# Optimization experiments

Measured on AMD Instinct MI355X. Metric: run time of the kernel, lower is better.

The kernel has to match this reference:

```python
import jax, jax.numpy as jnp
import numpy as np

N, S, D_MODEL, H = 2, 2048, 1024, 16
HEAD_DIM = D_MODEL // H


def setup_inputs() -> dict:
    key = jax.random.key(0)
    k1, k2, k3 = jax.random.split(key, 3)
    x = jax.random.normal(k1, (N, S, D_MODEL), dtype=jnp.float32)
    # Xavier-uniform-like scaling for the projection weights (torch layout: [out, in])
    lim_qkv = (6.0 / (D_MODEL + 3 * D_MODEL)) ** 0.5
    lim_o = (6.0 / (D_MODEL + D_MODEL)) ** 0.5
    qkv_w = jax.random.uniform(k2, (3 * D_MODEL, D_MODEL), dtype=jnp.float32, minval=-lim_qkv, maxval=lim_qkv)
    o_w = jax.random.uniform(k3, (D_MODEL, D_MODEL), dtype=jnp.float32, minval=-lim_o, maxval=lim_o)
    return {"x": x, "qkv_w": qkv_w, "o_w": o_w}


def reference(x, qkv_w, o_w):
    n, s, _ = x.shape
    # qkv projection (torch Linear: y = x @ W^T), no bias
    qkv = jnp.einsum("nsd,ed->nse", x, qkv_w)            # (N, S, 3*D_MODEL)
    qkv = qkv.reshape(n, s, H, 3 * HEAD_DIM).transpose(0, 2, 1, 3)  # (N, H, S, 3*hd)
    q, k, v = jnp.split(qkv, 3, axis=-1)                 # each (N, H, S, hd)
    scale = 1.0 / jnp.sqrt(jnp.float32(HEAD_DIM))
    attn_logits = jnp.einsum("nhqd,nhkd->nhqk", q, k) * scale  # (N, H, S, S)
    attn_weights = jax.nn.softmax(attn_logits, axis=-1)
    values = jnp.einsum("nhqk,nhkd->nhqd", attn_weights, v)    # (N, H, S, hd)
    values = values.transpose(0, 2, 1, 3).reshape(n, s, D_MODEL)
    o = jnp.einsum("nsd,ed->nse", values, o_w)           # (N, S, D_MODEL)
    return o
```

## Files before the change

### kernel.cpp

```cpp
#include <hip/hip_runtime.h>
#include <math.h>

#define H 16
#define S 2048
#define DM 1024
#define HD 64
#define QSCALE 0.18033688011112042f

typedef __attribute__((ext_vector_type(8))) short short8;
typedef __attribute__((ext_vector_type(4))) float f32x4;
typedef __attribute__((ext_vector_type(4))) unsigned short u16x4;
typedef __attribute__((ext_vector_type(2))) unsigned int uint2v;
#if __has_builtin(__builtin_amdgcn_cvt_pk_bf16_f32)
typedef __attribute__((ext_vector_type(2))) __bf16 bf16x2;
#endif

__device__ __forceinline__ unsigned short f2bf(float f) {
  unsigned int u = __builtin_bit_cast(unsigned int, f);
  u = (u + 0x7fffu + ((u >> 16) & 1u)) >> 16;
  return (unsigned short)u;
}

__device__ __forceinline__ unsigned int pk_bf16(float a, float b) {
#if __has_builtin(__builtin_amdgcn_cvt_pk_bf16_f32)
  bf16x2 r = __builtin_amdgcn_cvt_pk_bf16_f32(a, b);
  return __builtin_bit_cast(unsigned int, r);
#else
  return (unsigned int)f2bf(a) | ((unsigned int)f2bf(b) << 16);
#endif
}

__device__ __forceinline__ float fexp2(float x) {
#if __has_builtin(__builtin_amdgcn_exp2f)
  return __builtin_amdgcn_exp2f(x);
#else
  return exp2f(x);
#endif
}

__device__ __forceinline__ void async_ld16(const void* g, void* l) {
  __builtin_amdgcn_global_load_lds(
      (const __attribute__((address_space(1))) unsigned int*)g,
      (__attribute__((address_space(3))) unsigned int*)l, 16, 0, 0);
}

__global__ void detect_dtype(const unsigned int* __restrict__ x, int* __restrict__ flag) {
  unsigned int w0 = x[threadIdx.x];
  unsigned int e = (w0 >> 7) & 0xFFu;
  bool hit = (e >= 100u && e <= 140u);
  unsigned long long m = __ballot(hit);
  if (threadIdx.x == 0) *flag = (__popcll(m) >= 32) ? 1 : 0;
}

__global__ void convert_bf16(const void* __restrict__ in, unsigned short* __restrict__ out,
                             int n4, const int* __restrict__ flag) {
  int i = blockIdx.x * blockDim.x + threadIdx.x;
  if (i >= n4) return;
  u16x4 r;
  if (*flag == 0) {
    f32x4 v = ((const f32x4*)in)[i];
    r.x = f2bf(v.x); r.y = f2bf(v.y); r.z = f2bf(v.z); r.w = f2bf(v.w);
  } else {
    r = ((const u16x4*)in)[i];
  }
  ((u16x4*)out)[i] = r;
}

__global__ __launch_bounds__(256, 2) void gemm_qkv(
    const short* __restrict__ X, const short* __restrict__ W,
    unsigned short* __restrict__ qws, unsigned short* __restrict__ kws,
    unsigned short* __restrict__ vtws) {
  const int K = 1024;
  __shared__ __attribute__((aligned(16))) short As[128 * 64];
  __shared__ __attribute__((aligned(16))) short Bs[128 * 64];
  const int tid = threadIdx.x;
  const int w = tid >> 6, l = tid & 63, l15 = l & 15, quad = l >> 4;
  const int wm = (w >> 1) * 64, wn = (w & 1) * 64;
  const int row0 = blockIdx.y * 128, col0 = blockIdx.x * 128;

  f32x4 zero = {0.f, 0.f, 0.f, 0.f};
  f32x4 acc[4][4];
  for (int i = 0; i < 4; ++i)
    for (int j = 0; j < 4; ++j) acc[i][j] = zero;

  const short* Ag = X + row0 * K;
  const short* Bg = W + col0 * K;

  for (int k0 = 0; k0 < K; k0 += 64) {
    __syncthreads();
    for (int i = 0; i < 4; ++i) {
      int u = i * 256 + tid;
      int r = u >> 3, c = u & 7;
      async_ld16(Ag + r * K + k0 + c * 8, As + u * 8);
    }
    for (int i = 0; i < 4; ++i) {
      int u = i * 256 + tid;
      int r = u >> 3, c = u & 7;
      async_ld16(Bg + r * K + k0 + c * 8, Bs + u * 8);
    }
    __syncthreads();
    for (int kk = 0; kk < 2; ++kk) {
      short8 a[4], b[4];
      for (int i = 0; i < 4; ++i)
        a[i] = *(const short8*)(As + (wm + i * 16 + l15) * 64 + kk * 32 + quad * 8);
      for (int j = 0; j < 4; ++j)
        b[j] = *(const short8*)(Bs + (wn + j * 16 + l15) * 64 + kk * 32 + quad * 8);
      for (int i = 0; i < 4; ++i)
        for (int j = 0; j < 4; ++j)
          acc[i][j] = __builtin_amdgcn_mfma_f32_16x16x32_bf16(a[i], b[j], acc[i][j], 0, 0, 0);
    }
  }

  for (int i = 0; i < 4; ++i) {
    int rowb = row0 + wm + i * 16 + quad * 4;
    int n = rowb >> 11, s = rowb & 2047;
    for (int j = 0; j < 4; ++j) {
      int e = col0 + wn + j * 16 + l15;
      int h = e / 192;
      int rem = e - h * 192;
      int part = rem >> 6, d = rem & 63;
      f32x4 v = acc[i][j];
      if (part == 0) {
        unsigned short* p = qws + ((n * H + h) * S + s) * HD + d;
        p[0] = f2bf(v.x * QSCALE);
        p[HD] = f2bf(v.y * QSCALE);
        p[2 * HD] = f2bf(v.z * QSCALE);
        p[3 * HD] = f2bf(v.w * QSCALE);
      } else if (part == 1) {
        unsigned short* p = kws + ((n * H + h) * S + s) * HD + d;
        p[0] = f2bf(v.x);
        p[HD] = f2bf(v.y);
        p[2 * HD] = f2bf(v.z);
        p[3 * HD] = f2bf(v.w);
      } else {
        u16x4 pk;
        pk.x = f2bf(v.x); pk.y = f2bf(v.y); pk.z = f2bf(v.z); pk.w = f2bf(v.w);
        *(u16x4*)(vtws + ((n * H + h) * HD + d) * S + s) = pk;
      }
    }
  }
}

__global__ __launch_bounds__(256, 4) void flash(
    const short* __restrict__ qws, const short* __restrict__ kws,
    const short* __restrict__ vtws, unsigned short* __restrict__ vals) {
  __shared__ __attribute__((aligned(16))) short Ks[64 * 64];
  __shared__ __attribute__((aligned(16))) short Vts[64 * 64];
  __shared__ __attribute__((aligned(16))) short Pt[4][16 * 64];
  const int tid = threadIdx.x;
  const int w = tid >> 6, l = tid & 63, l15 = l & 15, quad = l >> 4;
  const int qb = blockIdx.x, h = blockIdx.y, n = blockIdx.z;
  const int nh = n * H + h;
  const short* Qh = qws + nh * S * HD;
  const short* Kh = kws + nh * S * HD;
  const short* Vth = vtws + nh * HD * S;

  const int q0 = qb * 64 + w * 16;
  short8 qf[2];
  for (int c = 0; c < 2; ++c)
    qf[c] = *(const short8*)(Qh + (q0 + l15) * HD + c * 32 + quad * 8);

  const int swz0 = ((4 * 0 + quad) ^ (l15 & 7)) * 8;
  const int swz1 = ((4 * 1 + quad) ^ (l15 & 7)) * 8;

  float lrun = 0.f;
  f32x4 zero = {0.f, 0.f, 0.f, 0.f};
  f32x4 oacc[4] = {zero, zero, zero, zero};

  for (int kv0 = 0; kv0 < S; kv0 += 64) {
    __syncthreads();
    for (int i = 0; i < 2; ++i) {
      int u = i * 256 + tid;
      int r = u >> 3, c = u & 7;
      int sw = r * 64 + ((c ^ (r & 7)) * 8);
      *(short8*)(Ks + sw) = *(const short8*)(Kh + (kv0 + r) * HD + c * 8);
      *(short8*)(Vts + sw) = *(const short8*)(Vth + r * S + kv0 + c * 8);
    }
    __syncthreads();

    f32x4 sacc[4] = {zero, zero, zero, zero};
    {
      short8 kf[4];
      for (int i = 0; i < 4; ++i)
        kf[i] = *(const short8*)(Ks + (i * 16 + l15) * 64 + swz0);
      for (int i = 0; i < 4; ++i)
        sacc[i] = __builtin_amdgcn_mfma_f32_16x16x32_bf16(kf[i], qf[0], sacc[i], 0, 0, 0);
      for (int i = 0; i < 4; ++i)
        kf[i] = *(const short8*)(Ks + (i * 16 + l15) * 64 + swz1);
      for (int i = 0; i < 4; ++i)
        sacc[i] = __builtin_amdgcn_mfma_f32_16x16x32_bf16(kf[i], qf[1], sacc[i], 0, 0, 0);
    }

    float rs = 0.f;
    for (int i = 0; i < 4; ++i) {
      f32x4 p;
      p.x = fexp2(sacc[i].x);
      p.y = fexp2(sacc[i].y);
      p.z = fexp2(sacc[i].z);
      p.w = fexp2(sacc[i].w);
      sacc[i] = p;
      rs += p.x + p.y + p.z + p.w;
    }
    rs += __shfl_xor(rs, 16);
    rs += __shfl_xor(rs, 32);
    lrun += rs;

    for (int i = 0; i < 4; ++i) {
      int g = 2 * i + (quad >> 1);
      uint2v pk;
      pk.x = pk_bf16(sacc[i].x, sacc[i].y);
      pk.y = pk_bf16(sacc[i].z, sacc[i].w);
      *(uint2v*)(&Pt[w][l15 * 64 + ((g ^ (l15 & 7)) * 8) + (quad & 1) * 4]) = pk;
    }
    asm volatile("s_waitcnt lgkmcnt(0)" ::: "memory");

    {
      short8 vf[4];
      short8 pf0 = *(const short8*)(&Pt[w][l15 * 64 + swz0]);
      short8 pf1 = *(const short8*)(&Pt[w][l15 * 64 + swz1]);
      for (int i = 0; i < 4; ++i)
        vf[i] = *(const short8*)(Vts + (i * 16 + l15) * 64 + swz0);
      for (int i = 0; i < 4; ++i)
        oacc[i] = __builtin_amdgcn_mfma_f32_16x16x32_bf16(vf[i], pf0, oacc[i], 0, 0, 0);
      for (int i = 0; i < 4; ++i)
        vf[i] = *(const short8*)(Vts + (i * 16 + l15) * 64 + swz1);
      for (int i = 0; i < 4; ++i)
        oacc[i] = __builtin_amdgcn_mfma_f32_16x16x32_bf16(vf[i], pf1, oacc[i], 0, 0, 0);
    }
  }

  float inv = 1.0f / lrun;
  int s = q0 + l15;
  for (int i = 0; i < 4; ++i) {
    uint2v pk;
    pk.x = pk_bf16(oacc[i].x * inv, oacc[i].y * inv);
    pk.y = pk_bf16(oacc[i].z * inv, oacc[i].w * inv);
    *(uint2v*)(vals + (n * S + s) * DM + h * HD + i * 16 + quad * 4) = pk;
  }
}

__global__ __launch_bounds__(256, 2) void gemm_out(
    const short* __restrict__ A, const short* __restrict__ W,
    float* __restrict__ out) {
  const int K = 1024;
  __shared__ __attribute__((aligned(16))) short As[128 * 64];
  __shared__ __attribute__((aligned(16))) short Bs[128 * 64];
  const int tid = threadIdx.x;
  const int w = tid >> 6, l = tid & 63, l15 = l & 15, quad = l >> 4;
  const int wm = (w >> 1) * 64, wn = (w & 1) * 64;
  const int row0 = blockIdx.y * 128, col0 = blockIdx.x * 128;

  f32x4 zero = {0.f, 0.f, 0.f, 0.f};
  f32x4 acc[4][4];
  for (int i = 0; i < 4; ++i)
    for (int j = 0; j < 4; ++j) acc[i][j] = zero;

  const short* Ag = A + row0 * K;
  const short* Bg = W + col0 * K;

  for (int k0 = 0; k0 < K; k0 += 64) {
    __syncthreads();
    for (int i = 0; i < 4; ++i) {
      int u = i * 256 + tid;
      int r = u >> 3, c = u & 7;
      async_ld16(Ag + r * K + k0 + c * 8, As + u * 8);
    }
    for (int i = 0; i < 4; ++i) {
      int u = i * 256 + tid;
      int r = u >> 3, c = u & 7;
      async_ld16(Bg + r * K + k0 + c * 8, Bs + u * 8);
    }
    __syncthreads();
    for (int kk = 0; kk < 2; ++kk) {
      short8 a[4], b[4];
      for (int i = 0; i < 4; ++i)
        a[i] = *(const short8*)(As + (wm + i * 16 + l15) * 64 + kk * 32 + quad * 8);
      for (int j = 0; j < 4; ++j)
        b[j] = *(const short8*)(Bs + (wn + j * 16 + l15) * 64 + kk * 32 + quad * 8);
      for (int i = 0; i < 4; ++i)
        for (int j = 0; j < 4; ++j)
          acc[i][j] = __builtin_amdgcn_mfma_f32_16x16x32_bf16(a[i], b[j], acc[i][j], 0, 0, 0);
    }
  }

  for (int i = 0; i < 4; ++i) {
    int rowb = row0 + wm + i * 16 + quad * 4;
    for (int j = 0; j < 4; ++j) {
      int e = col0 + wn + j * 16 + l15;
      f32x4 v = acc[i][j];
      out[(rowb + 0) * 1024 + e] = v.x;
      out[(rowb + 1) * 1024 + e] = v.y;
      out[(rowb + 2) * 1024 + e] = v.z;
      out[(rowb + 3) * 1024 + e] = v.w;
    }
  }
}

extern "C" void kernel_launch(void* const* d_in, const int* in_sizes, int n_in,
                              void* d_out, int out_size, void* d_ws, size_t ws_size,
                              hipStream_t stream) {
  const void* x = d_in[0];
  const void* qkv_w = d_in[1];
  const void* o_w = d_in[2];
  float* out = (float*)d_out;

  char* ws = (char*)d_ws;
  unsigned short* xb   = (unsigned short*)(ws);
  unsigned short* wb   = (unsigned short*)(ws + (8ull << 20));
  unsigned short* owb  = (unsigned short*)(ws + (14ull << 20));
  unsigned short* qws  = (unsigned short*)(ws + (16ull << 20));
  unsigned short* kws  = (unsigned short*)(ws + (24ull << 20));
  unsigned short* vtws = (unsigned short*)(ws + (32ull << 20));
  unsigned short* vals = xb;
  int* flag = (int*)(ws + (32ull << 20));

  detect_dtype<<<1, 64, 0, stream>>>((const unsigned int*)x, flag);
  convert_bf16<<<4096, 256, 0, stream>>>(x, xb, (2 * S * DM) / 4, flag);
  convert_bf16<<<3072, 256, 0, stream>>>(qkv_w, wb, (3 * DM * DM) / 4, flag);
  convert_bf16<<<1024, 256, 0, stream>>>(o_w, owb, (DM * DM) / 4, flag);

  gemm_qkv<<<dim3(24, 32), 256, 0, stream>>>(
      (const short*)xb, (const short*)wb, qws, kws, vtws);
  flash<<<dim3(32, 16, 2), 256, 0, stream>>>(
      (const short*)qws, (const short*)kws, (const short*)vtws, vals);
  gemm_out<<<dim3(8, 32), 256, 0, stream>>>(
      (const short*)vals, (const short*)owb, out);
}
```

Before: 204.5 us.

## Fuse conversion kernels, double-buffer flash K/V with async LDS loads

```diff
diff --git a/kernel.cpp b/kernel.cpp
--- a/kernel.cpp
+++ b/kernel.cpp
@@ -44,29 +44,29 @@
       (__attribute__((address_space(3))) unsigned int*)l, 16, 0, 0);
 }
 
-__global__ void detect_dtype(const unsigned int* __restrict__ x, int* __restrict__ flag) {
-  unsigned int w0 = x[threadIdx.x];
-  unsigned int e = (w0 >> 7) & 0xFFu;
-  bool hit = (e >= 100u && e <= 140u);
-  unsigned long long m = __ballot(hit);
-  if (threadIdx.x == 0) *flag = (__popcll(m) >= 32) ? 1 : 0;
-}
-
-__global__ void convert_bf16(const void* __restrict__ in, unsigned short* __restrict__ out,
-                             int n4, const int* __restrict__ flag) {
-  int i = blockIdx.x * blockDim.x + threadIdx.x;
-  if (i >= n4) return;
+__global__ void convert_all(const float* __restrict__ x, const float* __restrict__ w,
+                            const float* __restrict__ ow,
+                            unsigned short* __restrict__ xb,
+                            unsigned short* __restrict__ wb,
+                            unsigned short* __restrict__ owb) {
+  int b = blockIdx.x;
+  const f32x4* src;
+  u16x4* dst;
+  int idx;
+  if (b < 4096) {
+    src = (const f32x4*)x; dst = (u16x4*)xb; idx = b * 256 + threadIdx.x;
+  } else if (b < 7168) {
+    src = (const f32x4*)w; dst = (u16x4*)wb; idx = (b - 4096) * 256 + threadIdx.x;
+  } else {
+    src = (const f32x4*)ow; dst = (u16x4*)owb; idx = (b - 7168) * 256 + threadIdx.x;
+  }
+  f32x4 v = src[idx];
   u16x4 r;
-  if (*flag == 0) {
-    f32x4 v = ((const f32x4*)in)[i];
-    r.x = f2bf(v.x); r.y = f2bf(v.y); r.z = f2bf(v.z); r.w = f2bf(v.w);
-  } else {
-    r = ((const u16x4*)in)[i];
-  }
-  ((u16x4*)out)[i] = r;
-}
-
-__global__ __launch_bounds__(256, 2) void gemm_qkv(
+  r.x = f2bf(v.x); r.y = f2bf(v.y); r.z = f2bf(v.z); r.w = f2bf(v.w);
+  dst[idx] = r;
+}
+
+__global__ __launch_bounds__(256) void gemm_qkv(
     const short* __restrict__ X, const short* __restrict__ W,
     unsigned short* __restrict__ qws, unsigned short* __restrict__ kws,
     unsigned short* __restrict__ vtws) {
@@ -144,8 +144,8 @@
 __global__ __launch_bounds__(256, 4) void flash(
     const short* __restrict__ qws, const short* __restrict__ kws,
     const short* __restrict__ vtws, unsigned short* __restrict__ vals) {
-  __shared__ __attribute__((aligned(16))) short Ks[64 * 64];
-  __shared__ __attribute__((aligned(16))) short Vts[64 * 64];
+  __shared__ __attribute__((aligned(16))) short Ks[2][64 * 64];
+  __shared__ __attribute__((aligned(16))) short Vts[2][64 * 64];
   __shared__ __attribute__((aligned(16))) short Pt[4][16 * 64];
   const int tid = threadIdx.x;
   const int w = tid >> 6, l = tid & 63, l15 = l & 15, quad = l >> 4;
@@ -163,35 +163,42 @@
   const int swz0 = ((4 * 0 + quad) ^ (l15 & 7)) * 8;
   const int swz1 = ((4 * 1 + quad) ^ (l15 & 7)) * 8;
 
-  float lrun = 0.f;
+  float lpart = 0.f;
   f32x4 zero = {0.f, 0.f, 0.f, 0.f};
   f32x4 oacc[4] = {zero, zero, zero, zero};
 
-  for (int kv0 = 0; kv0 < S; kv0 += 64) {
-    __syncthreads();
+  auto stage = [&](int kv0, int buf) {
     for (int i = 0; i < 2; ++i) {
       int u = i * 256 + tid;
-      int r = u >> 3, c = u & 7;
-      int sw = r * 64 + ((c ^ (r & 7)) * 8);
-      *(short8*)(Ks + sw) = *(const short8*)(Kh + (kv0 + r) * HD + c * 8);
-      *(short8*)(Vts + sw) = *(const short8*)(Vth + r * S + kv0 + c * 8);
-    }
-    __syncthreads();
+      int r = u >> 3;
+      int c = (u & 7) ^ (r & 7);
+      async_ld16(Kh + (kv0 + r) * HD + c * 8, &Ks[buf][u * 8]);
+      async_ld16(Vth + r * S + kv0 + c * 8, &Vts[buf][u * 8]);
+    }
+  };
+
+  stage(0, 0);
+  for (int t = 0; t < 32; ++t) {
+    const int buf = t & 1;
+    __syncthreads();
+    if (t < 31) stage((t + 1) * 64, buf ^ 1);
+
+    const short* Kb = Ks[buf];
+    const short* Vb = Vts[buf];
 
     f32x4 sacc[4] = {zero, zero, zero, zero};
     {
       short8 kf[4];
       for (int i = 0; i < 4; ++i)
-        kf[i] = *(const short8*)(Ks + (i * 16 + l15) * 64 + swz0);
+        kf[i] = *(const short8*)(Kb + (i * 16 + l15) * 64 + swz0);
       for (int i = 0; i < 4; ++i)
         sacc[i] = __builtin_amdgcn_mfma_f32_16x16x32_bf16(kf[i], qf[0], sacc[i], 0, 0, 0);
       for (int i = 0; i < 4; ++i)
-        kf[i] = *(const short8*)(Ks + (i * 16 + l15) * 64 + swz1);
+        kf[i] = *(const short8*)(Kb + (i * 16 + l15) * 64 + swz1);
       for (int i = 0; i < 4; ++i)
         sacc[i] = __builtin_amdgcn_mfma_f32_16x16x32_bf16(kf[i], qf[1], sacc[i], 0, 0, 0);
     }
 
-    float rs = 0.f;
     for (int i = 0; i < 4; ++i) {
       f32x4 p;
       p.x = fexp2(sacc[i].x);
@@ -199,11 +206,8 @@
       p.z = fexp2(sacc[i].z);
       p.w = fexp2(sacc[i].w);
       sacc[i] = p;
-      rs += p.x + p.y + p.z + p.w;
-    }
-    rs += __shfl_xor(rs, 16);
-    rs += __shfl_xor(rs, 32);
-    lrun += rs;
+      lpart += p.x + p.y + p.z + p.w;
+    }
 
     for (int i = 0; i < 4; ++i) {
       int g = 2 * i + (quad >> 1);
@@ -219,16 +223,19 @@
       short8 pf0 = *(const short8*)(&Pt[w][l15 * 64 + swz0]);
       short8 pf1 = *(const short8*)(&Pt[w][l15 * 64 + swz1]);
       for (int i = 0; i < 4; ++i)
-        vf[i] = *(const short8*)(Vts + (i * 16 + l15) * 64 + swz0);
+        vf[i] = *(const short8*)(Vb + (i * 16 + l15) * 64 + swz0);
       for (int i = 0; i < 4; ++i)
         oacc[i] = __builtin_amdgcn_mfma_f32_16x16x32_bf16(vf[i], pf0, oacc[i], 0, 0, 0);
       for (int i = 0; i < 4; ++i)
-        vf[i] = *(const short8*)(Vts + (i * 16 + l15) * 64 + swz1);
+        vf[i] = *(const short8*)(Vb + (i * 16 + l15) * 64 + swz1);
       for (int i = 0; i < 4; ++i)
         oacc[i] = __builtin_amdgcn_mfma_f32_16x16x32_bf16(vf[i], pf1, oacc[i], 0, 0, 0);
     }
   }
 
+  float lrun = lpart;
+  lrun += __shfl_xor(lrun, 16);
+  lrun += __shfl_xor(lrun, 32);
   float inv = 1.0f / lrun;
   int s = q0 + l15;
   for (int i = 0; i < 4; ++i) {
@@ -239,7 +246,7 @@
   }
 }
 
-__global__ __launch_bounds__(256, 2) void gemm_out(
+__global__ __launch_bounds__(256) void gemm_out(
     const short* __restrict__ A, const short* __restrict__ W,
     float* __restrict__ out) {
   const int K = 1024;
@@ -299,9 +306,9 @@
 extern "C" void kernel_launch(void* const* d_in, const int* in_sizes, int n_in,
                               void* d_out, int out_size, void* d_ws, size_t ws_size,
                               hipStream_t stream) {
-  const void* x = d_in[0];
-  const void* qkv_w = d_in[1];
-  const void* o_w = d_in[2];
+  const float* x = (const float*)d_in[0];
+  const float* qkv_w = (const float*)d_in[1];
+  const float* o_w = (const float*)d_in[2];
   float* out = (float*)d_out;
 
   char* ws = (char*)d_ws;
@@ -312,13 +319,8 @@
   unsigned short* kws  = (unsigned short*)(ws + (24ull << 20));
   unsigned short* vtws = (unsigned short*)(ws + (32ull << 20));
   unsigned short* vals = xb;
-  int* flag = (int*)(ws + (32ull << 20));
-
-  detect_dtype<<<1, 64, 0, stream>>>((const unsigned int*)x, flag);
-  convert_bf16<<<4096, 256, 0, stream>>>(x, xb, (2 * S * DM) / 4, flag);
-  convert_bf16<<<3072, 256, 0, stream>>>(qkv_w, wb, (3 * DM * DM) / 4, flag);
-  convert_bf16<<<1024, 256, 0, stream>>>(o_w, owb, (DM * DM) / 4, flag);
-
+
+  convert_all<<<8192, 256, 0, stream>>>(x, qkv_w, o_w, xb, wb, owb);
   gemm_qkv<<<dim3(24, 32), 256, 0, stream>>>(
       (const short*)xb, (const short*)wb, qws, kws, vtws);
   flash<<<dim3(32, 16, 2), 256, 0, stream>>>(
```

After: 213.0 us. 4.1% more time.
